# Optimization experiments

Measured on AMD Instinct MI355X. Metric: run time of the kernel, lower is better.

Reference implementation:

```python
import jax, jax.numpy as jnp
import numpy as np

VOCAB = 100000
EMB = 20
HID = 10
SEQ = 100
NLAB = 15
BATCH = 16384


def setup_inputs() -> dict:
    key = jax.random.key(0)
    ks = jax.random.split(key, 7)
    x = jax.random.randint(ks[0], (BATCH, SEQ), 0, VOCAB, dtype=jnp.int32)
    embed_table = jax.random.normal(ks[1], (VOCAB, EMB), dtype=jnp.float32) * 0.05
    # Keras LSTMCell kernels: input kernel [EMB, 4H], recurrent kernel [HID, 4H], bias [4H]
    Wx = jax.random.normal(ks[2], (EMB, 4 * HID), dtype=jnp.float32) * (1.0 / np.sqrt(EMB))
    Wh = jax.random.normal(ks[3], (HID, 4 * HID), dtype=jnp.float32) * (1.0 / np.sqrt(HID))
    b = jnp.zeros((4 * HID,), dtype=jnp.float32).at[HID:2 * HID].set(1.0)  # unit forget bias
    Wd = jax.random.normal(ks[4], (HID, NLAB), dtype=jnp.float32) * (1.0 / np.sqrt(HID))
    bd = jnp.zeros((NLAB,), dtype=jnp.float32)
    return {"x": x, "embed_table": embed_table, "Wx": Wx, "Wh": Wh, "b": b,
            "Wd": Wd, "bd": bd, "drop_rate": 0}


def _lstm(e, Wx, Wh, b):
    # e: [B, T, E]. Precompute input projections for all steps at once.
    zx = jnp.einsum('bte,eg->btg', e, Wx) + b  # [B, T, 4H]
    B = e.shape[0]
    h0 = jnp.zeros((B, HID), dtype=e.dtype)
    c0 = jnp.zeros((B, HID), dtype=e.dtype)

    def step(carry, zx_t):
        h, c = carry
        z = zx_t + h @ Wh  # [B, 4H]
        zi, zf, zc, zo = jnp.split(z, 4, axis=-1)  # Keras gate order i,f,c,o
        i = jax.nn.sigmoid(zi)
        f = jax.nn.sigmoid(zf)
        o = jax.nn.sigmoid(zo)
        c_new = f * c + i * jnp.tanh(zc)
        h_new = o * jnp.tanh(c_new)
        return (h_new, c_new), None

    (hT, _), _ = jax.lax.scan(step, (h0, c0), jnp.swapaxes(zx, 0, 1))  # scan over time
    return hT  # [B, H]


def reference(x, embed_table, Wx, Wh, b, Wd, bd, drop_rate):
    e = embed_table[x]  # [B, T, E] embedding lookup
    h = _lstm(e, Wx, Wh, b)  # final hidden state, [B, H]
    # tf.nn.dropout with rate == drop_rate == 0 is an identity
    logits = h @ Wd + bd  # [B, NLAB]
    return logits
```

## Files before the change

### kernel.cpp

```cpp
#include <hip/hip_runtime.h>
#include <hip/hip_fp16.h>

#define VOCAB 100000
#define EMB   20
#define HID   10
#define SEQ   100
#define NLAB  15
#define BATCH 16384
#define GATES 40
#define PROWH 40

__device__ __forceinline__ float exp2_f(float x){ float r; asm("v_exp_f32 %0, %1" : "=v"(r) : "v"(x)); return r; }
__device__ __forceinline__ float rcp_f(float x){ float r; asm("v_rcp_f32 %0, %1" : "=v"(r) : "v"(x)); return r; }

__device__ __host__ __forceinline__ constexpr float gscale(int G){
  return (G == 2) ? -2.885390081777927f : -1.442695040888963f;
}

template<int OFF>
__device__ __forceinline__ float bswz(float x){
  return __int_as_float(__builtin_amdgcn_ds_swizzle(__float_as_int(x), OFF));
}

template<int CTRL>
__device__ __forceinline__ float qb(float x){
  return __int_as_float(__builtin_amdgcn_mov_dpp(__float_as_int(x), CTRL, 0xF, 0xF, true));
}

__global__ __launch_bounds__(256)
void proj_kernel_h(const float* __restrict__ emb, const float* __restrict__ Wx,
                   const float* __restrict__ bias, __half* __restrict__ P)
{
  __shared__ float Wxl[EMB * GATES];
  __shared__ float bl[GATES];
  const int tid = threadIdx.x;
  for (int i = tid; i < EMB * GATES; i += 256) {
    int k = i / GATES, slot = i - k * GATES;
    int u = slot >> 2, G = slot & 3;
    Wxl[i] = Wx[k * GATES + G * HID + u] * gscale(G);
  }
  if (tid < GATES) {
    int u = tid >> 2, G = tid & 3;
    bl[tid] = bias[G * HID + u] * gscale(G);
  }
  __syncthreads();

  const int v   = blockIdx.x * 32 + (tid >> 3);
  const int sub = tid & 7;
  if (v >= VOCAB) return;

  const float4* er = (const float4*)(emb + (size_t)v * EMB);
  float4 e0 = er[0], e1 = er[1], e2 = er[2], e3 = er[3], e4 = er[4];
  float e[EMB] = {e0.x,e0.y,e0.z,e0.w, e1.x,e1.y,e1.z,e1.w, e2.x,e2.y,e2.z,e2.w,
                  e3.x,e3.y,e3.z,e3.w, e4.x,e4.y,e4.z,e4.w};

  int sl[5] = {4*sub, 4*sub+1, 4*sub+2, 4*sub+3, 32+sub};
  float acc[5];
  #pragma unroll
  for (int c = 0; c < 5; ++c) acc[c] = bl[sl[c]];
  #pragma unroll
  for (int k = 0; k < EMB; ++k)
    #pragma unroll
    for (int c = 0; c < 5; ++c)
      acc[c] = fmaf(e[k], Wxl[k * GATES + sl[c]], acc[c]);

  union { __half h[4]; uint2 u2; } um;
  #pragma unroll
  for (int c = 0; c < 4; ++c) um.h[c] = __float2half(acc[c]);
  *(uint2*)(P + (size_t)v * PROWH + 4 * sub) = um.u2;
  P[(size_t)v * PROWH + 32 + sub] = __float2half(acc[4]);
}

__global__ __launch_bounds__(256, 2)
void rnn8h_kernel(const int* __restrict__ x, const __half* __restrict__ P,
                  const float* __restrict__ Wh, const float* __restrict__ Wd,
                  const float* __restrict__ bd, float* __restrict__ out)
{
  __shared__ int xs[32 * SEQ];
  const int tid = threadIdx.x;
  const int grp = tid >> 3;
  const int sub = tid & 7;
  const int b0  = blockIdx.x * 32;

  for (int i = tid; i < 32 * SEQ; i += 256) xs[i] = x[(size_t)b0 * SEQ + i];

  const int Ge = sub & 3;
  const int ue = 8 + (sub >> 2);
  float wm[HID][4], we[HID];
  #pragma unroll
  for (int k = 0; k < HID; ++k) {
    #pragma unroll
    for (int G = 0; G < 4; ++G)
      wm[k][G] = Wh[k * GATES + G * HID + sub] * gscale(G);
    we[k] = Wh[k * GATES + Ge * HID + ue] * gscale(Ge);
  }
  #pragma unroll
  for (int k = 0; k < HID; ++k) {
    #pragma unroll
    for (int G = 0; G < 4; ++G)
      asm volatile("" : "+v"(wm[k][G]));
    asm volatile("" : "+v"(we[k]));
  }

  __syncthreads();

  float cm = 0.f, cx = 0.f;
  float h[HID];
  #pragma unroll
  for (int k = 0; k < HID; ++k) h[k] = 0.f;

  const int* xrow = xs + grp * SEQ;

  uint2 mA, mB, mC; __half eA, eB, eC;
  auto ldrow = [&](uint2& m, __half& ex, int t) {
    int tt = t < SEQ ? t : SEQ - 1;
    const __half* rp = P + (size_t)xrow[tt] * PROWH;
    m  = *(const uint2*)(rp + 4 * sub);
    ex = rp[32 + sub];
  };
  ldrow(mA, eA, 0); ldrow(mB, eB, 1); ldrow(mC, eC, 2);

  auto step = [&](uint2& m, __half& ex, int t) {
    float zm[4], z5;
    {
      float2 a = __half22float2(*(const __half2*)&m.x);
      float2 b = __half22float2(*(const __half2*)&m.y);
      zm[0] = a.x; zm[1] = a.y; zm[2] = b.x; zm[3] = b.y;
      z5 = __half2float(ex);
    }
    ldrow(m, ex, t + 3);

    #pragma unroll
    for (int k = 0; k < HID; ++k) {
      #pragma unroll
      for (int G = 0; G < 4; ++G)
        zm[G] = fmaf(h[k], wm[k][G], zm[G]);
      z5 = fmaf(h[k], we[k], z5);
    }

    float zx0 = bswz<0x1C>(z5);
    float zx1 = bswz<0x3C>(z5);
    float zx2 = bswz<0x5C>(z5);
    float zx3 = bswz<0x7C>(z5);

    float hm;
    {
      float Ei = exp2_f(zm[0]);
      float Ef = exp2_f(zm[1]);
      float Ec = exp2_f(fminf(zm[2], 60.f));
      float Eo = exp2_f(zm[3]);
      float f  = rcp_f(1.f + Ef);
      float ig = (1.f - Ec) * rcp_f((1.f + Ei) * (1.f + Ec));
      cm = fmaf(f, cm, ig);
      float Et = exp2_f(fminf(-2.885390081777927f * cm, 60.f));
      hm = (1.f - Et) * rcp_f((1.f + Eo) * (1.f + Et));
    }
    float hx;
    {
      float Ei = exp2_f(zx0);
      float Ef = exp2_f(zx1);
      float Ec = exp2_f(fminf(zx2, 60.f));
      float Eo = exp2_f(zx3);
      float f  = rcp_f(1.f + Ef);
      float ig = (1.f - Ec) * rcp_f((1.f + Ei) * (1.f + Ec));
      cx = fmaf(f, cx, ig);
      float Et = exp2_f(fminf(-2.885390081777927f * cx, 60.f));
      hx = (1.f - Et) * rcp_f((1.f + Eo) * (1.f + Et));
    }

    h[0] = bswz<0x18>(hm); h[1] = bswz<0x38>(hm);
    h[2] = bswz<0x58>(hm); h[3] = bswz<0x78>(hm);
    h[4] = bswz<0x98>(hm); h[5] = bswz<0xB8>(hm);
    h[6] = bswz<0xD8>(hm); h[7] = bswz<0xF8>(hm);
    h[8] = bswz<0x18>(hx); h[9] = bswz<0x98>(hx);
  };

  #pragma unroll 1
  for (int t = 0; t < SEQ - 1; t += 3) {
    step(mA, eA, t);
    step(mB, eB, t + 1);
    step(mC, eC, t + 2);
  }
  step(mA, eA, SEQ - 1);

  #pragma unroll
  for (int s2 = 0; s2 < 2; ++s2) {
    int j = s2 * 8 + sub;
    if (j < NLAB) {
      float acc = bd[j];
      #pragma unroll
      for (int k = 0; k < HID; ++k)
        acc = fmaf(h[k], Wd[k * NLAB + j], acc);
      out[(size_t)(b0 + grp) * NLAB + j] = acc;
    }
  }
}

__global__ __launch_bounds__(256, 1)
void rnn_kernel_fb(const int* __restrict__ x, const float* __restrict__ emb,
                   const float* __restrict__ Wx, const float* __restrict__ Wh,
                   const float* __restrict__ bias, const float* __restrict__ Wd,
                   const float* __restrict__ bd, float* __restrict__ out)
{
  __shared__ int   xs[64 * SEQ];
  __shared__ float Wxl[EMB * 48];
  __shared__ float bls[48];
  const int tid = threadIdx.x, lb = tid >> 2, sub = tid & 3, b0 = blockIdx.x * 64;
  for (int i = tid; i < 64 * SEQ; i += 256) xs[i] = x[(size_t)b0 * SEQ + i];
  for (int i = tid; i < EMB * 48; i += 256) {
    int k = i / 48, slot = i - k * 48;
    int sb2 = slot / 12, r = slot - sb2 * 12, G = r / 3, s = r - G * 3, u = s * 4 + sb2;
    Wxl[i] = (u < HID) ? Wx[k * GATES + G * HID + u] * gscale(G) : 0.f;
  }
  if (tid < 48) {
    int slot = tid, sb2 = slot / 12, r = slot - sb2 * 12, G = r / 3, s = r - G * 3, u = s * 4 + sb2;
    bls[slot] = (u < HID) ? bias[G * HID + u] * gscale(G) : 0.f;
  }
  float Whr[HID][12];
  #pragma unroll
  for (int j = 0; j < 12; ++j) {
    const int G = j / 3, s = j - G * 3, u = s * 4 + sub;
    #pragma unroll
    for (int k = 0; k < HID; ++k)
      Whr[k][j] = (u < HID) ? Wh[k * GATES + G * HID + u] * gscale(G) : 0.f;
  }
  __syncthreads();
  float cst[3] = {0.f, 0.f, 0.f};
  float h[HID];
  #pragma unroll
  for (int k = 0; k < HID; ++k) h[k] = 0.f;
  float bb[12];
  #pragma unroll
  for (int j = 0; j < 12; ++j) bb[j] = bls[sub * 12 + j];
  const int* xrow = xs + lb * SEQ;
  float4 e0, e1, e2, e3, e4;
  {
    int row = xrow[0];
    const float4* q = (const float4*)(emb + (size_t)row * EMB);
    e0 = q[0]; e1 = q[1]; e2 = q[2]; e3 = q[3]; e4 = q[4];
  }
  #pragma unroll 1
  for (int t = 0; t < SEQ; ++t) {
    float e[EMB] = {e0.x,e0.y,e0.z,e0.w, e1.x,e1.y,e1.z,e1.w, e2.x,e2.y,e2.z,e2.w,
                    e3.x,e3.y,e3.z,e3.w, e4.x,e4.y,e4.z,e4.w};
    float z[12];
    #pragma unroll
    for (int j = 0; j < 12; ++j) z[j] = bb[j];
    #pragma unroll
    for (int k = 0; k < EMB; ++k)
      #pragma unroll
      for (int j = 0; j < 12; ++j)
        z[j] = fmaf(e[k], Wxl[k * 48 + sub * 12 + j], z[j]);
    if (t + 1 < SEQ) {
      int row = xrow[t + 1];
      const float4* q = (const float4*)(emb + (size_t)row * EMB);
      e0 = q[0]; e1 = q[1]; e2 = q[2]; e3 = q[3]; e4 = q[4];
    }
    #pragma unroll
    for (int k = 0; k < HID; ++k)
      #pragma unroll
      for (int j = 0; j < 12; ++j)
        z[j] = fmaf(h[k], Whr[k][j], z[j]);
    float hl[3];
    #pragma unroll
    for (int s = 0; s < 3; ++s) {
      float Ei = exp2_f(z[s]), Ef = exp2_f(z[s+3]);
      float Ec = exp2_f(fminf(z[s+6], 60.f)), Eo = exp2_f(z[s+9]);
      float f  = rcp_f(1.f + Ef);
      float ig = (1.f - Ec) * rcp_f((1.f + Ei) * (1.f + Ec));
      cst[s] = fmaf(f, cst[s], ig);
      float Et = exp2_f(fminf(-2.885390081777927f * cst[s], 60.f));
      hl[s] = (1.f - Et) * rcp_f((1.f + Eo) * (1.f + Et));
    }
    h[0] = qb<0x00>(hl[0]); h[1] = qb<0x55>(hl[0]); h[2] = qb<0xAA>(hl[0]); h[3] = qb<0xFF>(hl[0]);
    h[4] = qb<0x00>(hl[1]); h[5] = qb<0x55>(hl[1]); h[6] = qb<0xAA>(hl[1]); h[7] = qb<0xFF>(hl[1]);
    h[8] = qb<0x00>(hl[2]); h[9] = qb<0x55>(hl[2]);
  }
  #pragma unroll
  for (int s = 0; s < 4; ++s) {
    int j = s * 4 + sub;
    if (j < NLAB) {
      float acc = bd[j];
      #pragma unroll
      for (int k = 0; k < HID; ++k)
        acc = fmaf(h[k], Wd[k * NLAB + j], acc);
      out[(size_t)(b0 + lb) * NLAB + j] = acc;
    }
  }
}

extern "C" void kernel_launch(void* const* d_in, const int* in_sizes, int n_in,
                              void* d_out, int out_size, void* d_ws, size_t ws_size,
                              hipStream_t stream) {
  (void)in_sizes; (void)n_in; (void)out_size;
  const int*   x    = (const int*)  d_in[0];
  const float* emb  = (const float*)d_in[1];
  const float* Wx   = (const float*)d_in[2];
  const float* Wh   = (const float*)d_in[3];
  const float* bias = (const float*)d_in[4];
  const float* Wd   = (const float*)d_in[5];
  const float* bd   = (const float*)d_in[6];
  float* out = (float*)d_out;

  const size_t pbytes = (size_t)VOCAB * PROWH * sizeof(__half);
  if (ws_size >= pbytes) {
    __half* P = (__half*)d_ws;
    hipLaunchKernelGGL(proj_kernel_h, dim3((VOCAB + 31) / 32), dim3(256), 0, stream,
                       emb, Wx, bias, P);
    hipLaunchKernelGGL(rnn8h_kernel, dim3(BATCH / 32), dim3(256), 0, stream,
                       x, P, Wh, Wd, bd, out);
  } else {
    hipLaunchKernelGGL(rnn_kernel_fb, dim3(BATCH / 64), dim3(256), 0, stream,
                       x, emb, Wx, Wh, bias, Wd, bd, out);
  }
}
```

Before: 66.62 us.

## Use 16 lanes per sequence with LDS exchange of gates and hidden state

The recurrent kernel now gives each batch row 16 lanes instead of 8. Each lane computes two main gate pre-activations plus an extra-unit slot, writes them to a per-row shared-memory buffer, and reads back one unit's four gates as a float4. This drops the duplicated extra-unit cell math and ds_swizzle broadcasts, and halves the serial per-thread work on the time-step critical path. The cost is LDS round trips every step (relying on wavefront-synchronous ordering with no barrier), twice as many threads, and some lanes doing redundant gate work.

```diff
diff --git a/kernel.cpp b/kernel.cpp
--- a/kernel.cpp
+++ b/kernel.cpp
@@ -15,11 +15,6 @@
 
 __device__ __host__ __forceinline__ constexpr float gscale(int G){
   return (G == 2) ? -2.885390081777927f : -1.442695040888963f;
-}
-
-template<int OFF>
-__device__ __forceinline__ float bswz(float x){
-  return __int_as_float(__builtin_amdgcn_ds_swizzle(__float_as_int(x), OFF));
 }
 
 template<int CTRL>
@@ -71,108 +66,93 @@
   P[(size_t)v * PROWH + 32 + sub] = __float2half(acc[4]);
 }
 
-__global__ __launch_bounds__(256, 2)
-void rnn8h_kernel(const int* __restrict__ x, const __half* __restrict__ P,
+__global__ __launch_bounds__(256, 4)
+void rnn16_kernel(const int* __restrict__ x, const __half* __restrict__ P,
                   const float* __restrict__ Wh, const float* __restrict__ Wd,
                   const float* __restrict__ bd, float* __restrict__ out)
 {
-  __shared__ int xs[32 * SEQ];
+  __shared__ int xs[16 * SEQ];
+  __shared__ __align__(16) float zbuf[16][48];
+  __shared__ __align__(16) float hbuf[16][16];
+
   const int tid = threadIdx.x;
-  const int grp = tid >> 3;
-  const int sub = tid & 7;
-  const int b0  = blockIdx.x * 32;
-
-  for (int i = tid; i < 32 * SEQ; i += 256) xs[i] = x[(size_t)b0 * SEQ + i];
-
-  const int Ge = sub & 3;
-  const int ue = 8 + (sub >> 2);
-  float wm[HID][4], we[HID];
+  const int grp = tid >> 4;
+  const int L   = tid & 15;
+  const int b0  = blockIdx.x * 16;
+
+  for (int i = tid; i < 16 * SEQ; i += 256) xs[i] = x[(size_t)b0 * SEQ + i];
+
+  const int s0 = 2 * L, s1 = 2 * L + 1;
+  const int G0 = s0 & 3, u0 = s0 >> 2;
+  const int G1 = s1 & 3, u1 = s1 >> 2;
+  const int Ge = L & 3,  ue = 8 + (L >> 2);
+  float wm0[HID], wm1[HID], we[HID];
   #pragma unroll
   for (int k = 0; k < HID; ++k) {
-    #pragma unroll
-    for (int G = 0; G < 4; ++G)
-      wm[k][G] = Wh[k * GATES + G * HID + sub] * gscale(G);
-    we[k] = Wh[k * GATES + Ge * HID + ue] * gscale(Ge);
-  }
-  #pragma unroll
-  for (int k = 0; k < HID; ++k) {
-    #pragma unroll
-    for (int G = 0; G < 4; ++G)
-      asm volatile("" : "+v"(wm[k][G]));
-    asm volatile("" : "+v"(we[k]));
+    wm0[k] = Wh[k * GATES + G0 * HID + u0] * gscale(G0);
+    wm1[k] = Wh[k * GATES + G1 * HID + u1] * gscale(G1);
+    we[k]  = (L < 8) ? Wh[k * GATES + Ge * HID + ue] * gscale(Ge) : 0.f;
   }
 
   __syncthreads();
 
-  float cm = 0.f, cx = 0.f;
+  float* zrow = zbuf[grp];
+  float* hrow = hbuf[grp];
+  const int* xrow = xs + grp * SEQ;
+  const int ug = (L < 9) ? L : 9;
+
+  float cm = 0.f;
   float h[HID];
   #pragma unroll
   for (int k = 0; k < HID; ++k) h[k] = 0.f;
 
-  const int* xrow = xs + grp * SEQ;
-
-  uint2 mA, mB, mC; __half eA, eB, eC;
-  auto ldrow = [&](uint2& m, __half& ex, int t) {
+  unsigned mA, mB, mC; __half eA, eB, eC;
+  auto ldrow = [&](unsigned& m, __half& ex, int t) {
     int tt = t < SEQ ? t : SEQ - 1;
     const __half* rp = P + (size_t)xrow[tt] * PROWH;
-    m  = *(const uint2*)(rp + 4 * sub);
-    ex = rp[32 + sub];
+    m  = *(const unsigned*)(rp + 2 * L);
+    ex = rp[32 + (L & 7)];
   };
   ldrow(mA, eA, 0); ldrow(mB, eB, 1); ldrow(mC, eC, 2);
 
-  auto step = [&](uint2& m, __half& ex, int t) {
-    float zm[4], z5;
-    {
-      float2 a = __half22float2(*(const __half2*)&m.x);
-      float2 b = __half22float2(*(const __half2*)&m.y);
-      zm[0] = a.x; zm[1] = a.y; zm[2] = b.x; zm[3] = b.y;
-      z5 = __half2float(ex);
-    }
+  auto step = [&](unsigned& m, __half& ex, int t) {
+    float2 a = __half22float2(*(const __half2*)&m);
+    float z0 = a.x, z1 = a.y;
+    float z5 = __half2float(ex);
     ldrow(m, ex, t + 3);
 
     #pragma unroll
     for (int k = 0; k < HID; ++k) {
-      #pragma unroll
-      for (int G = 0; G < 4; ++G)
-        zm[G] = fmaf(h[k], wm[k][G], zm[G]);
-      z5 = fmaf(h[k], we[k], z5);
-    }
-
-    float zx0 = bswz<0x1C>(z5);
-    float zx1 = bswz<0x3C>(z5);
-    float zx2 = bswz<0x5C>(z5);
-    float zx3 = bswz<0x7C>(z5);
-
+      z0 = fmaf(h[k], wm0[k], z0);
+      z1 = fmaf(h[k], wm1[k], z1);
+      z5 = fmaf(h[k], we[k],  z5);
+    }
+
+    zrow[2 * L]     = z0;
+    zrow[2 * L + 1] = z1;
+    zrow[32 + L]    = z5;
+
+    const float4 g = *(const float4*)(zrow + 4 * ug);
     float hm;
     {
-      float Ei = exp2_f(zm[0]);
-      float Ef = exp2_f(zm[1]);
-      float Ec = exp2_f(fminf(zm[2], 60.f));
-      float Eo = exp2_f(zm[3]);
+      float Ei = exp2_f(g.x);
+      float Ef = exp2_f(g.y);
+      float Ec = exp2_f(fminf(g.z, 60.f));
+      float Eo = exp2_f(g.w);
       float f  = rcp_f(1.f + Ef);
       float ig = (1.f - Ec) * rcp_f((1.f + Ei) * (1.f + Ec));
       cm = fmaf(f, cm, ig);
       float Et = exp2_f(fminf(-2.885390081777927f * cm, 60.f));
       hm = (1.f - Et) * rcp_f((1.f + Eo) * (1.f + Et));
     }
-    float hx;
-    {
-      float Ei = exp2_f(zx0);
-      float Ef = exp2_f(zx1);
-      float Ec = exp2_f(fminf(zx2, 60.f));
-      float Eo = exp2_f(zx3);
-      float f  = rcp_f(1.f + Ef);
-      float ig = (1.f - Ec) * rcp_f((1.f + Ei) * (1.f + Ec));
-      cx = fmaf(f, cx, ig);
-      float Et = exp2_f(fminf(-2.885390081777927f * cx, 60.f));
-      hx = (1.f - Et) * rcp_f((1.f + Eo) * (1.f + Et));
-    }
-
-    h[0] = bswz<0x18>(hm); h[1] = bswz<0x38>(hm);
-    h[2] = bswz<0x58>(hm); h[3] = bswz<0x78>(hm);
-    h[4] = bswz<0x98>(hm); h[5] = bswz<0xB8>(hm);
-    h[6] = bswz<0xD8>(hm); h[7] = bswz<0xF8>(hm);
-    h[8] = bswz<0x18>(hx); h[9] = bswz<0x98>(hx);
+
+    hrow[L] = hm;
+    const float4 h03 = *(const float4*)(hrow);
+    const float4 h47 = *(const float4*)(hrow + 4);
+    const float2 h89 = *(const float2*)(hrow + 8);
+    h[0] = h03.x; h[1] = h03.y; h[2] = h03.z; h[3] = h03.w;
+    h[4] = h47.x; h[5] = h47.y; h[6] = h47.z; h[7] = h47.w;
+    h[8] = h89.x; h[9] = h89.y;
   };
 
   #pragma unroll 1
@@ -183,16 +163,12 @@
   }
   step(mA, eA, SEQ - 1);
 
-  #pragma unroll
-  for (int s2 = 0; s2 < 2; ++s2) {
-    int j = s2 * 8 + sub;
-    if (j < NLAB) {
-      float acc = bd[j];
-      #pragma unroll
-      for (int k = 0; k < HID; ++k)
-        acc = fmaf(h[k], Wd[k * NLAB + j], acc);
-      out[(size_t)(b0 + grp) * NLAB + j] = acc;
-    }
+  if (L < NLAB) {
+    float acc = bd[L];
+    #pragma unroll
+    for (int k = 0; k < HID; ++k)
+      acc = fmaf(h[k], Wd[k * NLAB + L], acc);
+    out[(size_t)(b0 + grp) * NLAB + L] = acc;
   }
 }
 
@@ -307,7 +283,7 @@
     __half* P = (__half*)d_ws;
     hipLaunchKernelGGL(proj_kernel_h, dim3((VOCAB + 31) / 32), dim3(256), 0, stream,
                        emb, Wx, bias, P);
-    hipLaunchKernelGGL(rnn8h_kernel, dim3(BATCH / 32), dim3(256), 0, stream,
+    hipLaunchKernelGGL(rnn16_kernel, dim3(BATCH / 16), dim3(256), 0, stream,
                        x, P, Wh, Wd, bd, out);
   } else {
     hipLaunchKernelGGL(rnn_kernel_fb, dim3(BATCH / 64), dim3(256), 0, stream,
```

After: 73.85 us. 10.8% more time.
